# Performance work log

Measured on AMD Instinct MI355X. Metric: run time of the kernel, lower is better.

The kernel has to match this reference:

```python
import jax, jax.numpy as jnp
import numpy as np

DIM, QK, PDIM = 384, 16, 96
EPS = 1e-5

def _bn(x, w, b, m, v):
    # eval-mode BatchNorm2d over channel axis 1 of [B,C,H,W]
    inv = w / jnp.sqrt(v + EPS)
    return x * inv[:, None, None] + (b - m * inv)[:, None, None]

def setup_inputs() -> dict:
    key = jax.random.key(0)
    ks = jax.random.split(key, 12)
    B, H, W = 64, 32, 32
    out_qkv = 2 * QK + PDIM  # 128
    return {
        "x": jax.random.normal(ks[0], (B, DIM, H, W), jnp.float32),
        "gn_w": jax.random.normal(ks[1], (PDIM,), jnp.float32) * 0.1 + 1.0,
        "gn_b": jax.random.normal(ks[2], (PDIM,), jnp.float32) * 0.1,
        "qkv_w": jax.random.normal(ks[3], (out_qkv, PDIM), jnp.float32) * 0.1,
        "qkv_bn_w": jax.random.normal(ks[4], (out_qkv,), jnp.float32) * 0.1 + 1.0,
        "qkv_bn_b": jax.random.normal(ks[5], (out_qkv,), jnp.float32) * 0.1,
        "qkv_bn_m": jax.random.normal(ks[6], (out_qkv,), jnp.float32) * 0.1,
        "qkv_bn_v": jax.random.uniform(ks[7], (out_qkv,), jnp.float32, 0.5, 1.5),
        "proj_w": jax.random.normal(ks[8], (DIM, DIM), jnp.float32) * 0.05,
        "proj_bn_w": jax.random.normal(ks[9], (DIM,), jnp.float32) * 0.1 + 1.0,
        "proj_bn_b": jax.random.normal(ks[10], (DIM,), jnp.float32) * 0.1,
        "proj_bn_m": jax.random.normal(ks[11], (DIM,), jnp.float32) * 0.1,
        "proj_bn_v": jax.random.uniform(jax.random.fold_in(key, 99), (DIM,), jnp.float32, 0.5, 1.5),
    }

def reference(x, gn_w, gn_b, qkv_w, qkv_bn_w, qkv_bn_b, qkv_bn_m, qkv_bn_v,
              proj_w, proj_bn_w, proj_bn_b, proj_bn_m, proj_bn_v):
    B, C, H, W = x.shape
    N = H * W
    scale = QK ** -0.5
    x1, x2 = x[:, :PDIM], x[:, PDIM:]
    # GroupNorm with 1 group: normalize over (C,H,W) per sample, per-channel affine
    mu = jnp.mean(x1, axis=(1, 2, 3), keepdims=True)
    var = jnp.var(x1, axis=(1, 2, 3), keepdims=True)
    x1n = (x1 - mu) * jax.lax.rsqrt(var + EPS)
    x1n = x1n * gn_w[:, None, None] + gn_b[:, None, None]
    # 1x1 conv (no bias) + eval BN
    qkv = jnp.einsum('oc,bchw->bohw', qkv_w, x1n)
    qkv = _bn(qkv, qkv_bn_w, qkv_bn_b, qkv_bn_m, qkv_bn_v)
    q = qkv[:, :QK].reshape(B, QK, N)
    k = qkv[:, QK:2 * QK].reshape(B, QK, N)
    v = qkv[:, 2 * QK:].reshape(B, PDIM, N)
    attn = jnp.einsum('bcn,bcm->bnm', q, k) * scale      # [B,N,N]
    attn = jax.nn.softmax(attn, axis=-1)
    x1o = jnp.einsum('bcm,bnm->bcn', v, attn).reshape(B, PDIM, H, W)
    y = jax.nn.silu(jnp.concatenate([x1o, x2], axis=1))
    y = jnp.einsum('oc,bchw->bohw', proj_w, y)
    return _bn(y, proj_bn_w, proj_bn_b, proj_bn_m, proj_bn_v)
```

## Files before the change

### kernel.cpp

```cpp
#include <hip/hip_runtime.h>

#define EPS 1e-5f

constexpr int B   = 64;
constexpr int DIM = 384;
constexpr int PD  = 96;
constexpr int QKD = 16;
constexpr int N   = 1024;
constexpr int OQ  = 128;
constexpr int Y2C = DIM - PD;
#define QSCALE 0.3606737602222408f

typedef __attribute__((ext_vector_type(8))) short bf16x8;
typedef __attribute__((ext_vector_type(16))) float f32x16;

#define MFMA(a, b, c) __builtin_amdgcn_mfma_f32_32x32x16_bf16((a), (b), (c), 0, 0, 0)

#define GLOAD16(gsrc, ldst)                                                    \
    __builtin_amdgcn_global_load_lds(                                          \
        (const __attribute__((address_space(1))) void*)(gsrc),                 \
        (__attribute__((address_space(3))) void*)(ldst), 16, 0, 0)

__device__ __forceinline__ unsigned short f2bf(float f) {
    union { float f; unsigned u; } v; v.f = f;
    unsigned r = v.u + 0x7fffu + ((v.u >> 16) & 1u);
    return (unsigned short)(r >> 16);
}
__device__ __forceinline__ unsigned pack2(float a, float b) {
    return (unsigned)f2bf(a) | ((unsigned)f2bf(b) << 16);
}
__device__ __forceinline__ unsigned cvtpk(float lo, float hi_) {
    unsigned r;
    asm("v_cvt_pk_bf16_f32 %0, %1, %2" : "=v"(r) : "v"(lo), "v"(hi_));
    return r;
}
__device__ __forceinline__ float max3f(float a, float b, float c) {
    return fmaxf(fmaxf(a, b), c);
}
__device__ __forceinline__ f32x16 zero16() {
    f32x16 z;
#pragma unroll
    for (int i = 0; i < 16; i++) z[i] = 0.f;
    return z;
}

__global__ __launch_bounds__(256) void k_pre(const float* __restrict__ x,
                                             float* __restrict__ part,
                                             const float* __restrict__ pw,
                                             const float* __restrict__ pbnw,
                                             const float* __restrict__ pbnb,
                                             const float* __restrict__ pbnm,
                                             const float* __restrict__ pbnv,
                                             short* __restrict__ Wp,
                                             float* __restrict__ bias,
                                             const float* __restrict__ qw,
                                             const float* __restrict__ qbnw,
                                             const float* __restrict__ qbnb,
                                             const float* __restrict__ qbnm,
                                             const float* __restrict__ qbnv,
                                             short* __restrict__ Wq,
                                             float* __restrict__ qbias) {
    __shared__ float r1[4], r2[4];
    int gb = blockIdx.x;
    int tid = threadIdx.x;
    if (gb < 512) {
        int b = gb >> 3, p = gb & 7;
        const float4* xp = (const float4*)(x + (size_t)b * DIM * N) + p * 3072;
        float s1a = 0.f, s1b = 0.f, s1c = 0.f, s1d = 0.f;
        float s2a = 0.f, s2b = 0.f, s2c = 0.f, s2d = 0.f;
        #pragma unroll
        for (int i = 0; i < 12; i += 4) {
            float4 v0 = xp[tid + (i + 0) * 256];
            float4 v1 = xp[tid + (i + 1) * 256];
            float4 v2 = xp[tid + (i + 2) * 256];
            float4 v3 = xp[tid + (i + 3) * 256];
            s1a += v0.x + v0.y + v0.z + v0.w;
            s2a += v0.x * v0.x + v0.y * v0.y + v0.z * v0.z + v0.w * v0.w;
            s1b += v1.x + v1.y + v1.z + v1.w;
            s2b += v1.x * v1.x + v1.y * v1.y + v1.z * v1.z + v1.w * v1.w;
            s1c += v2.x + v2.y + v2.z + v2.w;
            s2c += v2.x * v2.x + v2.y * v2.y + v2.z * v2.z + v2.w * v2.w;
            s1d += v3.x + v3.y + v3.z + v3.w;
            s2d += v3.x * v3.x + v3.y * v3.y + v3.z * v3.z + v3.w * v3.w;
        }
        float s1 = (s1a + s1b) + (s1c + s1d);
        float s2 = (s2a + s2b) + (s2c + s2d);
        for (int o = 32; o > 0; o >>= 1) {
            s1 += __shfl_down(s1, o, 64);
            s2 += __shfl_down(s2, o, 64);
        }
        int wave = tid >> 6, lane = tid & 63;
        if (lane == 0) { r1[wave] = s1; r2[wave] = s2; }
        __syncthreads();
        if (tid == 0) {
            part[(b * 8 + p) * 2 + 0] = r1[0] + r1[1] + r1[2] + r1[3];
            part[(b * 8 + p) * 2 + 1] = r2[0] + r2[1] + r2[2] + r2[3];
        }
    } else if (gb < 512 + 576) {
        int idx = (gb - 512) * 256 + tid;
        int o = idx / DIM;
        float inv = pbnw[o] * rsqrtf(pbnv[o] + EPS);
        Wp[idx] = (short)f2bf(pw[idx] * inv);
        if (idx < DIM) bias[idx] = pbnb[idx] - pbnm[idx] * (pbnw[idx] * rsqrtf(pbnv[idx] + EPS));
    } else {
        int idx = (gb - 1088) * 256 + tid;
        int o = idx / PD;
        float inv = qbnw[o] * rsqrtf(qbnv[o] + EPS);
        float f = (o < QKD) ? QSCALE : 1.f;
        Wq[idx] = (short)f2bf(qw[idx] * inv * f);
        if (idx < OQ) {
            float invb = qbnw[idx] * rsqrtf(qbnv[idx] + EPS);
            float fb = (idx < QKD) ? QSCALE : 1.f;
            qbias[idx] = (qbnb[idx] - qbnm[idx] * invb) * fb;
        }
    }
}

__global__ __launch_bounds__(256) void k_qkv(const float* __restrict__ x,
                                             const float* __restrict__ part,
                                             const float* __restrict__ gnw,
                                             const float* __restrict__ gnb,
                                             const short* __restrict__ Wq,
                                             const float* __restrict__ qbias,
                                             short* __restrict__ Qt,
                                             short* __restrict__ Kt,
                                             short* __restrict__ Vw) {
    alignas(16) __shared__ short Wl[128 * 104];
    alignas(16) __shared__ short Xl[128 * 104];
    __shared__ short t[32][132];
    __shared__ float qbl[OQ];
    __shared__ float pr[16];
    int b = blockIdx.x, nb = blockIdx.y;
    int tid = threadIdx.x, w = tid >> 6, l = tid & 63;
    int col = l & 31, hi = l >> 5;
    int wr = w >> 1, wc = w & 1;
    int n0 = nb * 128;

    if (tid < 16) pr[tid] = part[b * 16 + tid];
    if (tid >= 64 && tid < 64 + OQ) qbl[tid - 64] = qbias[tid - 64];
    #pragma unroll
    for (int it = 0; it < 6; it++) {
        int e = tid + 256 * it;
        int row = e / 12, slot = e % 12;
        *(uint4*)&Wl[row * 104 + slot * 8] = *(const uint4*)(Wq + row * PD + slot * 8);
    }
    __syncthreads();
    float s1 = (pr[0] + pr[2]) + (pr[4] + pr[6]) + (pr[8] + pr[10]) + (pr[12] + pr[14]);
    float s2 = (pr[1] + pr[3]) + (pr[5] + pr[7]) + (pr[9] + pr[11]) + (pr[13] + pr[15]);
    float mu = s1 / (PD * N);
    float var = s2 / (PD * N) - mu * mu;
    float rsig = rsqrtf(var + EPS);

    const float* xb = x + (size_t)b * DIM * N + n0;
    for (int ct = 0; ct < 3; ct++) {
        int c0 = ct * 32;
        if (ct) __syncthreads();
        #pragma unroll
        for (int i = 0; i < 4; i++) {
            int e = tid + 256 * i;
            int c = e >> 5, q4 = e & 31;
            float4 v = *(const float4*)(xb + (size_t)(c0 + c) * N + q4 * 4);
            float s = rsig * gnw[c0 + c];
            float tt = gnb[c0 + c] - mu * s;
            uint2 d;
            d.x = pack2(s * v.x + tt, s * v.y + tt);
            d.y = pack2(s * v.z + tt, s * v.w + tt);
            *(uint2*)&t[c][q4 * 4] = d;
        }
        __syncthreads();
        #pragma unroll
        for (int i = 0; i < 8; i++) {
            int e = tid + 256 * i;
            int n = e >> 4, cp = e & 15;
            unsigned lo = (unsigned short)t[2 * cp][n];
            unsigned hi2 = (unsigned short)t[2 * cp + 1][n];
            *(unsigned*)&Xl[n * 104 + c0 + 2 * cp] = lo | (hi2 << 16);
        }
    }
    __syncthreads();

    f32x16 acc[2][2];
    acc[0][0] = zero16(); acc[0][1] = zero16();
    acc[1][0] = zero16(); acc[1][1] = zero16();
    #pragma unroll
    for (int ks = 0; ks < 6; ks++) {
        int ko = ks * 16 + hi * 8;
        int ra0 = wr * 64 + col, ra1 = ra0 + 32;
        int rb0 = wc * 64 + col, rb1 = rb0 + 32;
        bf16x8 a0 = *(const bf16x8*)&Wl[ra0 * 104 + ko];
        bf16x8 a1 = *(const bf16x8*)&Wl[ra1 * 104 + ko];
        bf16x8 b0 = *(const bf16x8*)&Xl[rb0 * 104 + ko];
        bf16x8 b1 = *(const bf16x8*)&Xl[rb1 * 104 + ko];
        acc[0][0] = MFMA(a0, b0, acc[0][0]);
        acc[0][1] = MFMA(a0, b1, acc[0][1]);
        acc[1][0] = MFMA(a1, b0, acc[1][0]);
        acc[1][1] = MFMA(a1, b1, acc[1][1]);
    }

    #pragma unroll
    for (int m = 0; m < 2; m++) {
        int o_base = wr * 64 + m * 32;
        #pragma unroll
        for (int nn = 0; nn < 2; nn++) {
            int n = n0 + wc * 64 + nn * 32 + col;
            f32x16 a = acc[m][nn];
            if (o_base == 0) {
                #pragma unroll
                for (int g = 0; g < 4; g++) {
                    int ofr = 8 * g + 4 * hi;
                    float v0 = a[4 * g + 0] + qbl[ofr + 0];
                    float v1 = a[4 * g + 1] + qbl[ofr + 1];
                    float v2 = a[4 * g + 2] + qbl[ofr + 2];
                    float v3 = a[4 * g + 3] + qbl[ofr + 3];
                    uint2 d; d.x = pack2(v0, v1); d.y = pack2(v2, v3);
                    short* dst = (g < 2)
                        ? (Qt + ((size_t)b * N + n) * QKD + (ofr & 15))
                        : (Kt + ((size_t)b * N + n) * QKD + (ofr & 15));
                    *(uint2*)dst = d;
                }
            } else {
                int c0 = o_base - 32;
                short* vb = Vw + ((size_t)b * PD + c0) * N + n;
                #pragma unroll
                for (int r = 0; r < 16; r++) {
                    int cf = (r & 3) + 8 * (r >> 2) + 4 * hi;
                    vb[(size_t)cf * N] = (short)f2bf(a[r] + qbl[32 + c0 + cf]);
                }
            }
        }
    }
}

__global__ __launch_bounds__(512, 2) void k_attn(const short* __restrict__ Qt,
                                                 const short* __restrict__ Kt,
                                                 const short* __restrict__ Vb,
                                                 short* __restrict__ y1t) {
    alignas(16) __shared__ char lds_raw[4 * 96 * 72 * 2];
    short* Vs = (short*)lds_raw;
    float* combA_ = (float*)lds_raw;
    float* combM_ = (float*)(lds_raw + 50176);
    float* combL_ = (float*)(lds_raw + 51200);

    int b = blockIdx.x;
    int tid = threadIdx.x;
    int split = tid >> 8;
    int s_tid = tid & 255;
    int w = tid >> 6, lane = tid & 63;
    int qgrp = w & 3;
    int col = lane & 31, hi = lane >> 5;
    int q0 = blockIdx.y * 128 + qgrp * 32;
    int kbeg = split * 512;

    const short* kbase = Kt + (size_t)b * N * QKD;
    const short* vbase = Vb + (size_t)b * PD * N;
    const bf16x8 qf = *(const bf16x8*)(Qt + ((size_t)b * N + q0 + col) * QKD + hi * 8);

    short* vs0 = Vs + (split * 2 + 0) * (96 * 72);
    short* vs1 = Vs + (split * 2 + 1) * (96 * 72);

    bf16x8 kf0 = *(const bf16x8*)(kbase + (size_t)(kbeg + col) * QKD + hi * 8);
    bf16x8 kf1 = *(const bf16x8*)(kbase + (size_t)(kbeg + 32 + col) * QKD + hi * 8);
    {
        int t0 = s_tid, t1 = s_tid + 256, t2i = s_tid + 512;
        uint4 g0 = *(const uint4*)(vbase + (size_t)(t0 >> 3) * N + kbeg + (t0 & 7) * 8);
        uint4 g1 = *(const uint4*)(vbase + (size_t)(t1 >> 3) * N + kbeg + (t1 & 7) * 8);
        uint4 g2 = *(const uint4*)(vbase + (size_t)(t2i >> 3) * N + kbeg + (t2i & 7) * 8);
        *(uint4*)(vs0 + (t0 >> 3) * 72 + (t0 & 7) * 8) = g0;
        *(uint4*)(vs0 + (t1 >> 3) * 72 + (t1 & 7) * 8) = g1;
        *(uint4*)(vs0 + (t2i >> 3) * 72 + (t2i & 7) * 8) = g2;
    }
    __syncthreads();

    f32x16 acc0 = zero16(), acc1 = zero16(), acc2 = zero16();
    float m = -1e30f, lsum = 0.f;

    for (int it = 0; it < 8; it++) {
        int m0 = kbeg + it * 64;
        short* cur = (it & 1) ? vs1 : vs0;
        short* nxt = (it & 1) ? vs0 : vs1;
        bool more = (it < 7);
        int m0n = more ? m0 + 64 : m0;
        bf16x8 kf0n = *(const bf16x8*)(kbase + (size_t)(m0n + col) * QKD + hi * 8);
        bf16x8 kf1n = *(const bf16x8*)(kbase + (size_t)(m0n + 32 + col) * QKD + hi * 8);
        uint4 g0, g1, g2;
        if (more) {
            int t0 = s_tid, t1 = s_tid + 256, t2i = s_tid + 512;
            g0 = *(const uint4*)(vbase + (size_t)(t0 >> 3) * N + m0n + (t0 & 7) * 8);
            g1 = *(const uint4*)(vbase + (size_t)(t1 >> 3) * N + m0n + (t1 & 7) * 8);
            g2 = *(const uint4*)(vbase + (size_t)(t2i >> 3) * N + m0n + (t2i & 7) * 8);
        }

        f32x16 s0 = MFMA(kf0, qf, zero16());
        f32x16 s1 = MFMA(kf1, qf, zero16());
        float a0 = max3f(s0[0], s0[1], s0[2]),  a1 = max3f(s0[3], s0[4], s0[5]);
        float a2 = max3f(s0[6], s0[7], s0[8]),  a3 = max3f(s0[9], s0[10], s0[11]);
        float a4 = max3f(s0[12], s0[13], s0[14]);
        float cm0 = fmaxf(max3f(a0, a1, a2), max3f(a3, a4, s0[15]));
        float b0_ = max3f(s1[0], s1[1], s1[2]),  b1_ = max3f(s1[3], s1[4], s1[5]);
        float b2_ = max3f(s1[6], s1[7], s1[8]),  b3_ = max3f(s1[9], s1[10], s1[11]);
        float b4_ = max3f(s1[12], s1[13], s1[14]);
        float cm1 = fmaxf(max3f(b0_, b1_, b2_), max3f(b3_, b4_, s1[15]));
        float cm = fmaxf(cm0, cm1);
        cm = fmaxf(cm, __shfl_xor(cm, 32, 64));
        if (!__all(cm <= m + 8.f)) {
            float mnew = fmaxf(m, cm);
            float corr = __builtin_amdgcn_exp2f(m - mnew);
            m = mnew;
            lsum *= corr;
            #pragma unroll
            for (int r = 0; r < 16; r++) { acc0[r] *= corr; acc1[r] *= corr; acc2[r] *= corr; }
        }
        float ps = 0.f;
        bf16x8 pbv[2][2];
        #pragma unroll
        for (int s32 = 0; s32 < 2; s32++) {
            const f32x16& s = s32 ? s1 : s0;
            unsigned pw[8];
            #pragma unroll
            for (int j = 0; j < 8; j++) {
                float p0 = __builtin_amdgcn_exp2f(s[2 * j] - m);
                float p1 = __builtin_amdgcn_exp2f(s[2 * j + 1] - m);
                ps += p0 + p1;
                pw[j] = cvtpk(p0, p1);
            }
            unsigned xw[8];
            #pragma unroll
            for (int j = 0; j < 8; j++) xw[j] = __shfl_xor(pw[j], 32, 64);
            union { unsigned u[4]; bf16x8 v; } pb0, pb1;
            if (hi == 0) {
                pb0.u[0] = pw[0]; pb0.u[1] = pw[1]; pb0.u[2] = xw[0]; pb0.u[3] = xw[1];
                pb1.u[0] = pw[4]; pb1.u[1] = pw[5]; pb1.u[2] = xw[4]; pb1.u[3] = xw[5];
            } else {
                pb0.u[0] = xw[2]; pb0.u[1] = xw[3]; pb0.u[2] = pw[2]; pb0.u[3] = pw[3];
                pb1.u[0] = xw[6]; pb1.u[1] = xw[7]; pb1.u[2] = pw[6]; pb1.u[3] = pw[7];
            }
            pbv[s32][0] = pb0.v;
            pbv[s32][1] = pb1.v;
        }
        ps += __shfl_xor(ps, 32, 64);
        lsum += ps;
        __builtin_amdgcn_s_setprio(1);
        #pragma unroll
        for (int s32 = 0; s32 < 2; s32++) {
            const short* vt32 = cur + s32 * 32 + hi * 8;
            bf16x8 pa = pbv[s32][0], pq = pbv[s32][1];
            bf16x8 va0 = *(const bf16x8*)(vt32 + col * 72);
            bf16x8 va1 = *(const bf16x8*)(vt32 + col * 72 + 16);
            acc0 = MFMA(va0, pa, acc0);
            acc0 = MFMA(va1, pq, acc0);
            bf16x8 vb0 = *(const bf16x8*)(vt32 + (32 + col) * 72);
            bf16x8 vb1 = *(const bf16x8*)(vt32 + (32 + col) * 72 + 16);
            acc1 = MFMA(vb0, pa, acc1);
            acc1 = MFMA(vb1, pq, acc1);
            bf16x8 vc0 = *(const bf16x8*)(vt32 + (64 + col) * 72);
            bf16x8 vc1 = *(const bf16x8*)(vt32 + (64 + col) * 72 + 16);
            acc2 = MFMA(vc0, pa, acc2);
            acc2 = MFMA(vc1, pq, acc2);
        }
        __builtin_amdgcn_s_setprio(0);
        kf0 = kf0n; kf1 = kf1n;
        if (more) {
            int t0 = s_tid, t1 = s_tid + 256, t2i = s_tid + 512;
            *(uint4*)(nxt + (t0 >> 3) * 72 + (t0 & 7) * 8) = g0;
            *(uint4*)(nxt + (t1 >> 3) * 72 + (t1 & 7) * 8) = g1;
            *(uint4*)(nxt + (t2i >> 3) * 72 + (t2i & 7) * 8) = g2;
            __syncthreads();
        }
    }

    __syncthreads();
    if (split == 1) {
        float* dst = combA_ + (qgrp * 64 + lane) * 49;
        #pragma unroll
        for (int r = 0; r < 16; r++) {
            dst[r] = acc0[r]; dst[16 + r] = acc1[r]; dst[32 + r] = acc2[r];
        }
        combM_[qgrp * 64 + lane] = m;
        combL_[qgrp * 64 + lane] = lsum;
    }
    __syncthreads();
    if (split == 0) {
        float m2 = combM_[qgrp * 64 + lane], l2 = combL_[qgrp * 64 + lane];
        float M  = fmaxf(m, m2);
        float c1 = __builtin_amdgcn_exp2f(m - M);
        float c2 = __builtin_amdgcn_exp2f(m2 - M);
        float inv = 1.f / (lsum * c1 + l2 * c2);
        const float* src = combA_ + (qgrp * 64 + lane) * 49;
        float f1 = c1 * inv, f2 = c2 * inv;
        short* yrow = y1t + ((size_t)b * N + q0 + col) * PD;
        #pragma unroll
        for (int cg = 0; cg < 3; cg++) {
            f32x16 a = (cg == 0) ? acc0 : ((cg == 1) ? acc1 : acc2);
            const float* sr = src + cg * 16;
            #pragma unroll
            for (int j = 0; j < 8; j++) {
                float v0 = a[2 * j] * f1 + sr[2 * j] * f2;
                float v1 = a[2 * j + 1] * f1 + sr[2 * j + 1] * f2;
                v0 = v0 / (1.f + __expf(-v0));
                v1 = v1 / (1.f + __expf(-v1));
                int c = cg * 32 + ((2 * j) & 3) + 8 * (j >> 1) + 4 * hi;
                *(unsigned*)(yrow + c) = pack2(v0, v1);
            }
        }
    }
}

__global__ __launch_bounds__(256) void k_trans(const float* __restrict__ x,
                                               short* __restrict__ y2t) {
    int b = blockIdx.x, ct = blockIdx.y, nt = blockIdx.z;
    int tid = threadIdx.x;
    __shared__ short t[32][132];
    int c0 = PD + ct * 32, n0 = nt * 128;
    const float* xb = x + ((size_t)b * DIM + c0) * N + n0;
    #pragma unroll
    for (int i = 0; i < 4; i++) {
        int e = tid + 256 * i;
        int c = e >> 5, q4 = e & 31;
        float4 v = *(const float4*)(xb + (size_t)c * N + q4 * 4);
        float s0 = v.x / (1.f + __expf(-v.x));
        float s1 = v.y / (1.f + __expf(-v.y));
        float s2 = v.z / (1.f + __expf(-v.z));
        float s3 = v.w / (1.f + __expf(-v.w));
        uint2 d;
        d.x = pack2(s0, s1);
        d.y = pack2(s2, s3);
        *(uint2*)&t[c][q4 * 4] = d;
    }
    __syncthreads();
    #pragma unroll
    for (int i = 0; i < 8; i++) {
        int e = tid + 256 * i;
        int n = e >> 4, cp = e & 15;
        unsigned lo = (unsigned short)t[2 * cp][n];
        unsigned hi = (unsigned short)t[2 * cp + 1][n];
        *(unsigned*)(y2t + ((size_t)b * N + n0 + n) * Y2C + ct * 32 + 2 * cp) = lo | (hi << 16);
    }
}

__global__ __launch_bounds__(256) void k_proj(const short* __restrict__ Wp,
                                              const short* __restrict__ y1t,
                                              const short* __restrict__ y2t,
                                              const float* __restrict__ bias,
                                              float* __restrict__ out) {
    __shared__ short Asl[128 * 32];
    __shared__ short Bsl[128 * 32];
    int b = blockIdx.x, ob = blockIdx.y, nb = blockIdx.z;
    int tid = threadIdx.x, w = tid >> 6, l = tid & 63;
    int col = l & 31, hi = l >> 5;
    int wr = w >> 1, wc = w & 1;
    int o0 = ob * 128, n0 = nb * 128;
    size_t bn = (size_t)b * N + n0;

    f32x16 acc[2][2];
    acc[0][0] = zero16(); acc[0][1] = zero16();
    acc[1][0] = zero16(); acc[1][1] = zero16();

    int srow = (l >> 2);
    int sslotbase = (l & 3);

    for (int step = 0; step < 12; step++) {
        int k0 = step * 32;
        const short* ysrc;
        int ystride, kq;
        if (k0 < PD) { ysrc = y1t; ystride = PD;  kq = k0; }
        else         { ysrc = y2t; ystride = Y2C; kq = k0 - PD; }
        #pragma unroll
        for (int i = 0; i < 2; i++) {
            int row = w * 32 + i * 16 + srow;
            int sl = sslotbase ^ (row & 3);
            GLOAD16(Wp + (size_t)(o0 + row) * DIM + k0 + sl * 8,
                    &Asl[(w * 32 + i * 16) * 32]);
            GLOAD16(ysrc + (bn + row) * ystride + kq + sl * 8,
                    &Bsl[(w * 32 + i * 16) * 32]);
        }
        __syncthreads();
        #pragma unroll
        for (int kh = 0; kh < 2; kh++) {
            int bxor = ((kh << 5) + (hi << 4));
            int ra0 = wr * 64 + col,      ra1 = ra0 + 32;
            int rb0 = wc * 64 + col,      rb1 = rb0 + 32;
            bf16x8 a0 = *(const bf16x8*)&Asl[ra0 * 32 + ((bxor ^ ((ra0 & 3) << 4)) >> 1)];
            bf16x8 a1 = *(const bf16x8*)&Asl[ra1 * 32 + ((bxor ^ ((ra1 & 3) << 4)) >> 1)];
            bf16x8 b0 = *(const bf16x8*)&Bsl[rb0 * 32 + ((bxor ^ ((rb0 & 3) << 4)) >> 1)];
            bf16x8 b1 = *(const bf16x8*)&Bsl[rb1 * 32 + ((bxor ^ ((rb1 & 3) << 4)) >> 1)];
            acc[0][0] = MFMA(a0, b0, acc[0][0]);
            acc[0][1] = MFMA(a0, b1, acc[0][1]);
            acc[1][0] = MFMA(a1, b0, acc[1][0]);
            acc[1][1] = MFMA(a1, b1, acc[1][1]);
        }
        __syncthreads();
    }
    #pragma unroll
    for (int m = 0; m < 2; m++) {
        #pragma unroll
        for (int n = 0; n < 2; n++) {
            #pragma unroll
            for (int r = 0; r < 16; r++) {
                int o = o0 + wr * 64 + m * 32 + (r & 3) + 8 * (r >> 2) + 4 * hi;
                out[((size_t)b * DIM + o) * N + n0 + wc * 64 + n * 32 + col] =
                    acc[m][n][r] + bias[o];
            }
        }
    }
}

extern "C" void kernel_launch(void* const* d_in, const int* in_sizes, int n_in,
                              void* d_out, int out_size, void* d_ws, size_t ws_size,
                              hipStream_t stream) {
    const float* x    = (const float*)d_in[0];
    const float* gnw  = (const float*)d_in[1];
    const float* gnb  = (const float*)d_in[2];
    const float* qkvw = (const float*)d_in[3];
    const float* qbnw = (const float*)d_in[4];
    const float* qbnb = (const float*)d_in[5];
    const float* qbnm = (const float*)d_in[6];
    const float* qbnv = (const float*)d_in[7];
    const float* pw   = (const float*)d_in[8];
    const float* pbnw = (const float*)d_in[9];
    const float* pbnb = (const float*)d_in[10];
    const float* pbnm = (const float*)d_in[11];
    const float* pbnv = (const float*)d_in[12];
    float* out = (float*)d_out;

    char* p = (char*)d_ws;
    float* part  = (float*)p;  p += 4096;
    short* Wp    = (short*)p;  p += (size_t)DIM * DIM * 2;
    float* bias  = (float*)p;  p += 1536;
    short* Wq    = (short*)p;  p += (size_t)OQ * PD * 2;
    float* qbias = (float*)p;  p += 512;
    short* y1t   = (short*)p;  p += (size_t)B * N * PD * 2;
    short* Qt    = (short*)p;
    short* Kt    = Qt + (size_t)B * N * QKD;
    short* Vw    = Kt + (size_t)B * N * QKD;
    short* y2t   = Qt;

    k_pre<<<1136, 256, 0, stream>>>(x, part, pw, pbnw, pbnb, pbnm, pbnv, Wp, bias,
                                    qkvw, qbnw, qbnb, qbnm, qbnv, Wq, qbias);
    k_qkv<<<dim3(B, 8), 256, 0, stream>>>(x, part, gnw, gnb, Wq, qbias, Qt, Kt, Vw);
    k_attn<<<dim3(B, 8), 512, 0, stream>>>(Qt, Kt, Vw, y1t);
    k_trans<<<dim3(B, 9, 8), 256, 0, stream>>>(x, y2t);
    k_proj<<<dim3(B, 3, 8), 256, 0, stream>>>(Wp, y1t, y2t, bias, out);
}
```

Measured before the change: 107.8 us.

## Fuse silu-transpose of passthrough channels into projection GEMM B-tile loading

Removes the separate transpose kernel that wrote SiLU'd bf16 x2 to a workspace. The projection GEMM now reads fp32 x directly for K steps beyond the attention channels, applies SiLU, and transposes through shared memory into the swizzled B tile. This saves a launch and an intermediate write/read, but each output-channel block re-reads x and recomputes SiLU, adds extra barriers and LDS, and uses synchronous loads instead of async LDS loads.

```diff
diff --git a/kernel.cpp b/kernel.cpp
--- a/kernel.cpp
+++ b/kernel.cpp
@@ -8,7 +8,6 @@
 constexpr int QKD = 16;
 constexpr int N   = 1024;
 constexpr int OQ  = 128;
-constexpr int Y2C = DIM - PD;
 #define QSCALE 0.3606737602222408f
 
 typedef __attribute__((ext_vector_type(8))) short bf16x8;
@@ -405,45 +404,14 @@
     }
 }
 
-__global__ __launch_bounds__(256) void k_trans(const float* __restrict__ x,
-                                               short* __restrict__ y2t) {
-    int b = blockIdx.x, ct = blockIdx.y, nt = blockIdx.z;
-    int tid = threadIdx.x;
-    __shared__ short t[32][132];
-    int c0 = PD + ct * 32, n0 = nt * 128;
-    const float* xb = x + ((size_t)b * DIM + c0) * N + n0;
-    #pragma unroll
-    for (int i = 0; i < 4; i++) {
-        int e = tid + 256 * i;
-        int c = e >> 5, q4 = e & 31;
-        float4 v = *(const float4*)(xb + (size_t)c * N + q4 * 4);
-        float s0 = v.x / (1.f + __expf(-v.x));
-        float s1 = v.y / (1.f + __expf(-v.y));
-        float s2 = v.z / (1.f + __expf(-v.z));
-        float s3 = v.w / (1.f + __expf(-v.w));
-        uint2 d;
-        d.x = pack2(s0, s1);
-        d.y = pack2(s2, s3);
-        *(uint2*)&t[c][q4 * 4] = d;
-    }
-    __syncthreads();
-    #pragma unroll
-    for (int i = 0; i < 8; i++) {
-        int e = tid + 256 * i;
-        int n = e >> 4, cp = e & 15;
-        unsigned lo = (unsigned short)t[2 * cp][n];
-        unsigned hi = (unsigned short)t[2 * cp + 1][n];
-        *(unsigned*)(y2t + ((size_t)b * N + n0 + n) * Y2C + ct * 32 + 2 * cp) = lo | (hi << 16);
-    }
-}
-
 __global__ __launch_bounds__(256) void k_proj(const short* __restrict__ Wp,
                                               const short* __restrict__ y1t,
-                                              const short* __restrict__ y2t,
+                                              const float* __restrict__ x,
                                               const float* __restrict__ bias,
                                               float* __restrict__ out) {
     __shared__ short Asl[128 * 32];
     __shared__ short Bsl[128 * 32];
+    __shared__ short t[32][132];
     int b = blockIdx.x, ob = blockIdx.y, nb = blockIdx.z;
     int tid = threadIdx.x, w = tid >> 6, l = tid & 63;
     int col = l & 31, hi = l >> 5;
@@ -460,20 +428,48 @@
 
     for (int step = 0; step < 12; step++) {
         int k0 = step * 32;
-        const short* ysrc;
-        int ystride, kq;
-        if (k0 < PD) { ysrc = y1t; ystride = PD;  kq = k0; }
-        else         { ysrc = y2t; ystride = Y2C; kq = k0 - PD; }
         #pragma unroll
         for (int i = 0; i < 2; i++) {
             int row = w * 32 + i * 16 + srow;
             int sl = sslotbase ^ (row & 3);
             GLOAD16(Wp + (size_t)(o0 + row) * DIM + k0 + sl * 8,
                     &Asl[(w * 32 + i * 16) * 32]);
-            GLOAD16(ysrc + (bn + row) * ystride + kq + sl * 8,
-                    &Bsl[(w * 32 + i * 16) * 32]);
-        }
-        __syncthreads();
+        }
+        if (k0 < PD) {
+            #pragma unroll
+            for (int i = 0; i < 2; i++) {
+                int row = w * 32 + i * 16 + srow;
+                int sl = sslotbase ^ (row & 3);
+                GLOAD16(y1t + (bn + row) * PD + k0 + sl * 8,
+                        &Bsl[(w * 32 + i * 16) * 32]);
+            }
+            __syncthreads();
+        } else {
+            const float* xb2 = x + ((size_t)b * DIM + k0) * N + n0;
+            #pragma unroll
+            for (int i = 0; i < 4; i++) {
+                int e = tid + 256 * i;
+                int c = e >> 5, q4 = e & 31;
+                float4 v = *(const float4*)(xb2 + (size_t)c * N + q4 * 4);
+                float s0 = v.x / (1.f + __expf(-v.x));
+                float s1 = v.y / (1.f + __expf(-v.y));
+                float s2 = v.z / (1.f + __expf(-v.z));
+                float s3 = v.w / (1.f + __expf(-v.w));
+                uint2 d; d.x = pack2(s0, s1); d.y = pack2(s2, s3);
+                *(uint2*)&t[c][q4 * 4] = d;
+            }
+            __syncthreads();
+            #pragma unroll
+            for (int i = 0; i < 8; i++) {
+                int e = tid + 256 * i;
+                int n = e >> 4, cp = e & 15;
+                unsigned lo = (unsigned short)t[2 * cp][n];
+                unsigned hi2 = (unsigned short)t[2 * cp + 1][n];
+                int bo = (4 * cp) ^ ((n & 3) << 4);
+                *(unsigned*)((char*)Bsl + n * 64 + bo) = lo | (hi2 << 16);
+            }
+            __syncthreads();
+        }
         #pragma unroll
         for (int kh = 0; kh < 2; kh++) {
             int bxor = ((kh << 5) + (hi << 4));
@@ -529,15 +525,13 @@
     short* Wq    = (short*)p;  p += (size_t)OQ * PD * 2;
     float* qbias = (float*)p;  p += 512;
     short* y1t   = (short*)p;  p += (size_t)B * N * PD * 2;
-    short* Qt    = (short*)p;
-    short* Kt    = Qt + (size_t)B * N * QKD;
-    short* Vw    = Kt + (size_t)B * N * QKD;
-    short* y2t   = Qt;
+    short* Qt    = (short*)p;  p += (size_t)B * N * QKD * 2;
+    short* Kt    = (short*)p;  p += (size_t)B * N * QKD * 2;
+    short* Vw    = (short*)p;
 
     k_pre<<<1136, 256, 0, stream>>>(x, part, pw, pbnw, pbnb, pbnm, pbnv, Wp, bias,
                                     qkvw, qbnw, qbnb, qbnm, qbnv, Wq, qbias);
     k_qkv<<<dim3(B, 8), 256, 0, stream>>>(x, part, gnw, gnb, Wq, qbias, Qt, Kt, Vw);
     k_attn<<<dim3(B, 8), 512, 0, stream>>>(Qt, Kt, Vw, y1t);
-    k_trans<<<dim3(B, 9, 8), 256, 0, stream>>>(x, y2t);
-    k_proj<<<dim3(B, 3, 8), 256, 0, stream>>>(Wp, y1t, y2t, bias, out);
-}
+    k_proj<<<dim3(B, 3, 8), 256, 0, stream>>>(Wp, y1t, x, bias, out);
+}
```

Result: slower. 122.0 us (+13.1%).
